# Kernel optimization log

Measured on AMD Instinct MI355X. Metric: run time of the kernel, lower is better.

The kernel has to match this reference:

```python
import jax, jax.numpy as jnp
import numpy as np
import math

H = 16  # num heads
NEG = -1e9


def setup_inputs() -> dict:
    key = jax.random.key(0)
    ks = jax.random.split(key, 12)
    B, S, D = 2, 2048, 1024
    inp = {
        "query": jax.random.normal(ks[0], (B, S, D), jnp.float32),
        "key": jax.random.normal(ks[1], (B, S, D), jnp.float32),
        "value": jax.random.normal(ks[2], (B, S, D), jnp.float32),
        "mask": jax.random.randint(ks[3], (B, 1, S), 0, 2, jnp.int32),
        "wq": jax.random.normal(ks[4], (D, D), jnp.float32) * 0.02,
        "bq": jnp.zeros((D,), jnp.float32),
        "wk": jax.random.normal(ks[5], (D, D), jnp.float32) * 0.02,
        "bk": jnp.zeros((D,), jnp.float32),
        "wv": jax.random.normal(ks[6], (D, D), jnp.float32) * 0.02,
        "bv": jnp.zeros((D,), jnp.float32),
        "wo": jax.random.normal(ks[7], (D, D), jnp.float32) * 0.02,
        "bo": jnp.zeros((D,), jnp.float32),
    }
    return inp


def reference(query, key, value, mask, wq, bq, wk, bk, wv, bv, wo, bo):
    B, S, D = query.shape
    dk = D // H

    def proj(x, w, b):
        # torch Linear: x @ w.T + b ; then split heads -> [B, H, S, dk]
        y = x @ w.T + b
        return y.reshape(B, -1, H, dk).transpose(0, 2, 1, 3)

    q = proj(query, wq, bq)
    k = proj(key, wk, bk)
    v = proj(value, wv, bv)

    scores = jnp.einsum("bhqd,bhkd->bhqk", q, k) / math.sqrt(dk)  # [B,H,S,S]

    m = mask[:, None, :, :]  # [B,1,1,S] (mask.unsqueeze(1) in torch)
    scores = jnp.where(m == 0, NEG, scores)            # key-side padding mask
    scores = jnp.where(jnp.swapaxes(m, -2, -1) == 0, NEG, scores)  # query-side mask (q_len>1)

    p_attn = jax.nn.softmax(scores, axis=-1)
    # dropout p=0 / eval mode -> identity
    ctx = jnp.einsum("bhqk,bhkd->bhqd", p_attn, v)  # [B,H,S,dk]
    ctx = ctx.transpose(0, 2, 1, 3).reshape(B, S, H * dk)
    out = ctx @ wo.T + bo
    return out
```

## Files before the change

### kernel.cpp

```cpp
#include <hip/hip_runtime.h>
#include <hip/hip_bf16.h>

#define SEQ 2048
#define DIM 1024
#define NH  16
#define DK  64
#define NA  (2 * SEQ * DIM)
#define NW  (DIM * DIM)
#define PSTR 72
#define ESTR 136
#define FSTR 132
#define QSCALE 0.18033688011112042f

typedef __attribute__((ext_vector_type(4))) float f32x4;
typedef __attribute__((ext_vector_type(8))) __bf16 bf16x8;
typedef __attribute__((ext_vector_type(4))) __bf16 bf16x4;

__device__ __forceinline__ f32x4 mfma16(bf16x8 a, bf16x8 b, f32x4 c) {
  return __builtin_amdgcn_mfma_f32_16x16x32_bf16(a, b, c, 0, 0, 0);
}
__device__ __forceinline__ void async_load16(const void* g, void* l) {
  __builtin_amdgcn_global_load_lds(
      (const __attribute__((address_space(1))) void*)g,
      (__attribute__((address_space(3))) void*)l, 16, 0, 0);
}
__device__ __forceinline__ int swz(int row, int chunk) {
  return row * 8 + (chunk ^ (row & 7));
}

__global__ __launch_bounds__(256) void cvt_kernel(
    const float* __restrict__ s0, const float* __restrict__ s1,
    const float* __restrict__ s2, const float* __restrict__ s3,
    const float* __restrict__ s4, const float* __restrict__ s5,
    const float* __restrict__ s6,
    __hip_bfloat16* __restrict__ d0, __hip_bfloat16* __restrict__ d1,
    __hip_bfloat16* __restrict__ d2, __hip_bfloat16* __restrict__ d3,
    __hip_bfloat16* __restrict__ d4, __hip_bfloat16* __restrict__ d5,
    __hip_bfloat16* __restrict__ d6) {
  const int id = blockIdx.x;
  const float* s;
  __hip_bfloat16* d;
  int bid;
  if (id < 6144) {
    int t = id >> 11;
    bid = id & 2047;
    s = (t == 0) ? s0 : ((t == 1) ? s1 : s2);
    d = (t == 0) ? d0 : ((t == 1) ? d1 : d2);
  } else {
    int t = (id - 6144) >> 9;
    bid = (id - 6144) & 511;
    s = (t == 0) ? s3 : ((t == 1) ? s4 : ((t == 2) ? s5 : s6));
    d = (t == 0) ? d3 : ((t == 1) ? d4 : ((t == 2) ? d5 : d6));
  }
  size_t i = ((size_t)bid * 256 + threadIdx.x) * 8;
  float4 a = *(const float4*)(s + i);
  float4 b = *(const float4*)(s + i + 4);
  bf16x8 v = {(__bf16)a.x, (__bf16)a.y, (__bf16)a.z, (__bf16)a.w,
              (__bf16)b.x, (__bf16)b.y, (__bf16)b.z, (__bf16)b.w};
  *(bf16x8*)(d + i) = v;
}

__device__ __forceinline__ void gemm_stage(
    const __hip_bfloat16* __restrict__ X, const __hip_bfloat16* __restrict__ W,
    __hip_bfloat16* A, __hip_bfloat16* B, int m0, int n0, int k0,
    int w, int lane) {
  for (int r = 0; r < 4; ++r) {
    int cbase = r * 256 + w * 64;
    int c = cbase + lane, row = c >> 3, cs = c & 7;
    int off = cs ^ (row & 7);
    async_load16((const char*)(X + (size_t)(m0 + row) * DIM + k0) + off * 16,
                 (char*)A + cbase * 16);
    async_load16((const char*)(W + (size_t)(n0 + row) * DIM + k0) + off * 16,
                 (char*)B + cbase * 16);
  }
}

__device__ __forceinline__ void gemm_mainloop(
    const __hip_bfloat16* __restrict__ X, const __hip_bfloat16* __restrict__ W,
    __hip_bfloat16* lds, int m0, int n0, f32x4 acc[4][4]) {
  const int tid = threadIdx.x, lane = tid & 63, w = tid >> 6;
  const int quad = lane >> 4, l15 = lane & 15;
  const int wm = (w >> 1) * 64, wn = (w & 1) * 64;

  f32x4 z = {0.f, 0.f, 0.f, 0.f};
  for (int mi = 0; mi < 4; ++mi)
    for (int ni = 0; ni < 4; ++ni) acc[mi][ni] = z;

  gemm_stage(X, W, lds, lds + 8192, m0, n0, 0, w, lane);
  __syncthreads();

  for (int it = 0; it < 16; ++it) {
    __hip_bfloat16* Ac = lds + (it & 1) * 16384;
    __hip_bfloat16* Bc = Ac + 8192;
    if (it < 15) {
      __hip_bfloat16* An = lds + ((it + 1) & 1) * 16384;
      gemm_stage(X, W, An, An + 8192, m0, n0, (it + 1) * 64, w, lane);
    }
    for (int kk = 0; kk < 2; ++kk) {
      bf16x8 a[4], b[4];
      for (int mi = 0; mi < 4; ++mi)
        a[mi] = *(const bf16x8*)(Ac + swz(wm + mi * 16 + l15, kk * 4 + quad) * 8);
      for (int ni = 0; ni < 4; ++ni)
        b[ni] = *(const bf16x8*)(Bc + swz(wn + ni * 16 + l15, kk * 4 + quad) * 8);
      for (int mi = 0; mi < 4; ++mi)
        for (int ni = 0; ni < 4; ++ni)
          acc[mi][ni] = mfma16(a[mi], b[ni], acc[mi][ni]);
    }
    __syncthreads();
  }
}

__global__ __launch_bounds__(256) void qkv_proj_kernel(
    const __hip_bfloat16* __restrict__ xq, const __hip_bfloat16* __restrict__ xk,
    const __hip_bfloat16* __restrict__ xv,
    const __hip_bfloat16* __restrict__ wq, const __hip_bfloat16* __restrict__ wk,
    const __hip_bfloat16* __restrict__ wv,
    const float* __restrict__ bq, const float* __restrict__ bk,
    const float* __restrict__ bv,
    __hip_bfloat16* __restrict__ q_ws, __hip_bfloat16* __restrict__ k_ws,
    __hip_bfloat16* __restrict__ vt_ws) {
  __shared__ __align__(16) __hip_bfloat16 S_lds[4 * 8192];

  const int z = blockIdx.z;
  const __hip_bfloat16* X = (z == 0) ? xq : ((z == 1) ? xk : xv);
  const __hip_bfloat16* W = (z == 0) ? wq : ((z == 1) ? wk : wv);
  const float* bias = (z == 0) ? bq : ((z == 1) ? bk : bv);
  const float f = (z == 0) ? QSCALE : 1.0f;

  const int m0 = blockIdx.y * 128, n0 = blockIdx.x * 128;
  f32x4 acc[4][4];
  gemm_mainloop(X, W, S_lds, m0, n0, acc);

  const int tid = threadIdx.x, lane = tid & 63, w = tid >> 6;
  const int quad = lane >> 4, l15 = lane & 15;
  const int wm = (w >> 1) * 64, wn = (w & 1) * 64;

  if (z != 2) {
    __hip_bfloat16* out = (z == 0) ? q_ws : k_ws;
    for (int mi = 0; mi < 4; ++mi)
      for (int ni = 0; ni < 4; ++ni) {
        const float bv_ = bias[n0 + wn + ni * 16 + l15];
        for (int r = 0; r < 4; ++r)
          S_lds[(wm + mi * 16 + quad * 4 + r) * ESTR + wn + ni * 16 + l15] =
              __float2bfloat16((acc[mi][ni][r] + bv_) * f);
      }
    __syncthreads();
    for (int r2 = 0; r2 < 8; ++r2) {
      int c = r2 * 256 + tid;
      int row = c >> 4, j = c & 15;
      int m = m0 + row, b = m >> 11, s = m & 2047;
      int n = n0 + j * 8, h = n >> 6, d = n & 63;
      *(uint4*)(out + ((size_t)(b * NH + h) * SEQ + s) * DK + d) =
          *(const uint4*)(S_lds + row * ESTR + j * 8);
    }
  } else {
    for (int mi = 0; mi < 4; ++mi)
      for (int ni = 0; ni < 4; ++ni) {
        const int n_local = wn + ni * 16 + l15;
        const float bv_ = bias[n0 + n_local];
        bf16x4 tv;
        for (int r = 0; r < 4; ++r) tv[r] = (__bf16)(acc[mi][ni][r] + bv_);
        *(bf16x4*)(S_lds + n_local * ESTR + wm + mi * 16 + quad * 4) = tv;
      }
    __syncthreads();
    const int b = m0 >> 11, s_base = m0 & 2047;
    for (int r2 = 0; r2 < 8; ++r2) {
      int c2 = r2 * 256 + tid;
      int nrow = c2 >> 4, moff = (c2 & 15) * 8;
      int n = n0 + nrow, h = n >> 6, d = n & 63;
      *(uint4*)(vt_ws + ((size_t)(b * NH + h) * DK + d) * SEQ + s_base + moff) =
          *(const uint4*)(S_lds + nrow * ESTR + moff);
    }
  }
}

__global__ __launch_bounds__(256) void attn_kernel(
    const __hip_bfloat16* __restrict__ qg, const __hip_bfloat16* __restrict__ kg,
    const __hip_bfloat16* __restrict__ vtg, const int* __restrict__ mask,
    __hip_bfloat16* __restrict__ ctx) {
  __shared__ __align__(16) __hip_bfloat16 QP_lds[128 * PSTR];
  __shared__ __align__(16) __hip_bfloat16 K_lds[2][64 * 64];
  __shared__ __align__(16) __hip_bfloat16 V_lds[2][64 * 64];
  __shared__ float bias_lds[SEQ];

  const int tid = threadIdx.x, lane = tid & 63, w = tid >> 6;
  const int quad = lane >> 4, l15 = lane & 15;
  const int bh = blockIdx.y, b = bh >> 4, h = bh & 15;
  const int q0 = blockIdx.x * 128;
  const size_t head = (size_t)bh * SEQ * DK;
  const size_t vthead = (size_t)bh * DK * SEQ;

  for (int i = tid; i < SEQ; i += 256)
    bias_lds[i] = mask[b * SEQ + i] ? 0.f : -1e9f;

  for (int r = 0; r < 4; ++r) {
    int cbase = r * 256 + w * 64;
    int c = cbase + lane, row = c >> 3, cs = c & 7;
    int off = cs ^ (row & 7);
    async_load16((const char*)(qg + head + (size_t)(q0 + row) * DK) + off * 16,
                 (char*)QP_lds + cbase * 16);
  }
  for (int r = 0; r < 2; ++r) {
    int cbase = r * 256 + w * 64;
    int c = cbase + lane, row = c >> 3, cs = c & 7;
    int off = cs ^ (row & 7);
    async_load16((const char*)(kg + head + (size_t)row * DK) + off * 16,
                 (char*)K_lds[0] + cbase * 16);
    async_load16((const char*)(vtg + vthead + (size_t)row * SEQ) + off * 16,
                 (char*)V_lds[0] + cbase * 16);
  }
  __syncthreads();

  bf16x8 qf[2][2];
  for (int kk = 0; kk < 2; ++kk)
    for (int ni = 0; ni < 2; ++ni)
      qf[kk][ni] = *(const bf16x8*)(QP_lds + swz(w * 32 + ni * 16 + l15, kk * 4 + quad) * 8);
  int qmv[2];
  for (int ni = 0; ni < 2; ++ni)
    qmv[ni] = mask[b * SEQ + q0 + w * 32 + ni * 16 + l15];

  __hip_bfloat16* P_lds = QP_lds;
  const bf16x8 ones = {(__bf16)1.f, (__bf16)1.f, (__bf16)1.f, (__bf16)1.f,
                       (__bf16)1.f, (__bf16)1.f, (__bf16)1.f, (__bf16)1.f};

  f32x4 z = {0.f, 0.f, 0.f, 0.f};
  f32x4 o_acc[2][4];
  for (int ni = 0; ni < 2; ++ni)
    for (int di = 0; di < 4; ++di) o_acc[ni][di] = z;
  f32x4 o_sum[2] = {z, z};

  for (int t = 0; t < 32; ++t) {
    const int cur = t & 1;
    if (t < 31) {
      const int k1 = (t + 1) * 64;
      for (int r = 0; r < 2; ++r) {
        int cbase = r * 256 + w * 64;
        int c = cbase + lane, row = c >> 3, cs = c & 7;
        int off = cs ^ (row & 7);
        async_load16((const char*)(kg + head + (size_t)(k1 + row) * DK) + off * 16,
                     (char*)K_lds[1 - cur] + cbase * 16);
        async_load16((const char*)(vtg + vthead + (size_t)row * SEQ + k1) + off * 16,
                     (char*)V_lds[1 - cur] + cbase * 16);
      }
    }
    const int k0 = t * 64;

    f32x4 s_acc[4][2];
    for (int mi = 0; mi < 4; ++mi) {
      f32x4 kb = *(const f32x4*)(bias_lds + k0 + mi * 16 + quad * 4);
      for (int ni = 0; ni < 2; ++ni) s_acc[mi][ni] = kb;
    }
    for (int kk = 0; kk < 2; ++kk) {
      bf16x8 ak[4];
      for (int mi = 0; mi < 4; ++mi)
        ak[mi] = *(const bf16x8*)(K_lds[cur] + swz(mi * 16 + l15, kk * 4 + quad) * 8);
      for (int mi = 0; mi < 4; ++mi)
        for (int ni = 0; ni < 2; ++ni)
          s_acc[mi][ni] = mfma16(ak[mi], qf[kk][ni], s_acc[mi][ni]);
    }

    for (int mi = 0; mi < 4; ++mi)
      for (int ni = 0; ni < 2; ++ni) {
        bf16x4 pk;
        for (int r = 0; r < 4; ++r) {
          float s2 = qmv[ni] ? s_acc[mi][ni][r] : 0.f;
          pk[r] = (__bf16)__builtin_amdgcn_exp2f(s2);
        }
        *(bf16x4*)(P_lds + (w * 32 + ni * 16 + l15) * PSTR + mi * 16 + quad * 4) = pk;
      }

    for (int kk = 0; kk < 2; ++kk) {
      bf16x8 av[4], bp[2];
      for (int di = 0; di < 4; ++di)
        av[di] = *(const bf16x8*)(V_lds[cur] + swz(di * 16 + l15, kk * 4 + quad) * 8);
      for (int ni = 0; ni < 2; ++ni)
        bp[ni] = *(const bf16x8*)(P_lds + (w * 32 + ni * 16 + l15) * PSTR + kk * 32 + quad * 8);
      for (int ni = 0; ni < 2; ++ni) {
        for (int di = 0; di < 4; ++di)
          o_acc[ni][di] = mfma16(av[di], bp[ni], o_acc[ni][di]);
        o_sum[ni] = mfma16(ones, bp[ni], o_sum[ni]);
      }
    }
    __syncthreads();
  }

  const float inv[2] = {1.f / o_sum[0][0], 1.f / o_sum[1][0]};

  for (int ni = 0; ni < 2; ++ni)
    for (int di = 0; di < 4; ++di) {
      bf16x4 ov;
      for (int r = 0; r < 4; ++r) ov[r] = (__bf16)(o_acc[ni][di][r] * inv[ni]);
      *(bf16x4*)(P_lds + (w * 32 + ni * 16 + l15) * PSTR + di * 16 + quad * 4) = ov;
    }
  __syncthreads();
  for (int r = 0; r < 4; ++r) {
    int c = r * 256 + tid, row = c >> 3, off = c & 7;
    *(uint4*)(ctx + (size_t)(b * SEQ + q0 + row) * DIM + h * DK + off * 8) =
        *(const uint4*)(P_lds + row * PSTR + off * 8);
  }
}

__global__ __launch_bounds__(256) void out_proj_kernel(
    const __hip_bfloat16* __restrict__ ctx, const __hip_bfloat16* __restrict__ wo,
    const float* __restrict__ bo, float* __restrict__ out) {
  __shared__ __align__(16) char S_raw[128 * FSTR * 4];
  __hip_bfloat16* S_lds = (__hip_bfloat16*)S_raw;

  const int m0 = blockIdx.y * 128, n0 = blockIdx.x * 128;
  f32x4 acc[4][4];
  gemm_mainloop(ctx, wo, S_lds, m0, n0, acc);

  const int tid = threadIdx.x, lane = tid & 63, w = tid >> 6;
  const int quad = lane >> 4, l15 = lane & 15;
  const int wm = (w >> 1) * 64, wn = (w & 1) * 64;
  float* epi = (float*)S_raw;

  for (int mi = 0; mi < 4; ++mi)
    for (int ni = 0; ni < 4; ++ni) {
      const float bv_ = bo[n0 + wn + ni * 16 + l15];
      for (int r = 0; r < 4; ++r)
        epi[(wm + mi * 16 + quad * 4 + r) * FSTR + wn + ni * 16 + l15] =
            acc[mi][ni][r] + bv_;
    }
  __syncthreads();
  for (int r2 = 0; r2 < 16; ++r2) {
    int c = r2 * 256 + tid;
    int row = c >> 5, j = c & 31;
    *(float4*)(out + (size_t)(m0 + row) * DIM + n0 + j * 4) =
        *(const float4*)(epi + row * FSTR + j * 4);
  }
}

extern "C" void kernel_launch(void* const* d_in, const int* in_sizes, int n_in,
                              void* d_out, int out_size, void* d_ws, size_t ws_size,
                              hipStream_t stream) {
  const float* query = (const float*)d_in[0];
  const float* key   = (const float*)d_in[1];
  const float* value = (const float*)d_in[2];
  const int*   mask  = (const int*)d_in[3];
  const float* wq = (const float*)d_in[4];
  const float* bq = (const float*)d_in[5];
  const float* wk = (const float*)d_in[6];
  const float* bk = (const float*)d_in[7];
  const float* wv = (const float*)d_in[8];
  const float* bv = (const float*)d_in[9];
  const float* wo = (const float*)d_in[10];
  const float* bo = (const float*)d_in[11];
  float* out = (float*)d_out;

  char* ws = (char*)d_ws;
  const size_t SZA = (size_t)NA * 2;
  const size_t SZW = (size_t)NW * 2;
  __hip_bfloat16* xq  = (__hip_bfloat16*)(ws);
  __hip_bfloat16* xk  = (__hip_bfloat16*)(ws + SZA);
  __hip_bfloat16* xv  = (__hip_bfloat16*)(ws + 2 * SZA);
  __hip_bfloat16* wqb = (__hip_bfloat16*)(ws + 3 * SZA);
  __hip_bfloat16* wkb = (__hip_bfloat16*)(ws + 3 * SZA + SZW);
  __hip_bfloat16* wvb = (__hip_bfloat16*)(ws + 3 * SZA + 2 * SZW);
  __hip_bfloat16* wob = (__hip_bfloat16*)(ws + 3 * SZA + 3 * SZW);
  __hip_bfloat16* q_ws  = (__hip_bfloat16*)(ws + 3 * SZA + 4 * SZW);
  __hip_bfloat16* k_ws  = (__hip_bfloat16*)(ws + 4 * SZA + 4 * SZW);
  __hip_bfloat16* vt_ws = (__hip_bfloat16*)(ws + 5 * SZA + 4 * SZW);
  __hip_bfloat16* ctx_ws = xq;

  cvt_kernel<<<dim3(8192), dim3(256), 0, stream>>>(
      query, key, value, wq, wk, wv, wo, xq, xk, xv, wqb, wkb, wvb, wob);
  qkv_proj_kernel<<<dim3(8, 32, 3), dim3(256), 0, stream>>>(
      xq, xk, xv, wqb, wkb, wvb, bq, bk, bv, q_ws, k_ws, vt_ws);
  attn_kernel<<<dim3(16, 32), dim3(256), 0, stream>>>(q_ws, k_ws, vt_ws, mask, ctx_ws);
  out_proj_kernel<<<dim3(8, 32), dim3(256), 0, stream>>>(ctx_ws, wob, bo, out);
}
```

Before: 243.4 us.

## Split attention KV range across two wave halves with LDS reduction

The attention block grows to 512 threads. Each pair of waves handles the same 32 query rows, and each wave in the pair takes one half of the key sequence, so partial outputs and row sums are combined through LDS at the end. The mask-to-bias conversion moves into an extra block of the conversion kernel and is read from global memory, and Q fragments are loaded directly from global instead of staged through LDS. The aim is more waves in flight per block for better latency hiding. In exchange, the K/V double buffering is dropped in favour of a load-then-sync per iteration, which exposes load latency and adds a reduction step.

Result: faster. 223.3 us (-8.2%).

```diff
diff --git a/kernel.cpp b/kernel.cpp
--- a/kernel.cpp
+++ b/kernel.cpp
@@ -32,12 +32,17 @@
     const float* __restrict__ s0, const float* __restrict__ s1,
     const float* __restrict__ s2, const float* __restrict__ s3,
     const float* __restrict__ s4, const float* __restrict__ s5,
-    const float* __restrict__ s6,
+    const float* __restrict__ s6, const int* __restrict__ mask,
     __hip_bfloat16* __restrict__ d0, __hip_bfloat16* __restrict__ d1,
     __hip_bfloat16* __restrict__ d2, __hip_bfloat16* __restrict__ d3,
     __hip_bfloat16* __restrict__ d4, __hip_bfloat16* __restrict__ d5,
-    __hip_bfloat16* __restrict__ d6) {
+    __hip_bfloat16* __restrict__ d6, float* __restrict__ biasg) {
   const int id = blockIdx.x;
+  if (id == 8192) {
+    for (int i = threadIdx.x; i < 2 * SEQ; i += 256)
+      biasg[i] = mask[i] ? 0.f : -1e9f;
+    return;
+  }
   const float* s;
   __hip_bfloat16* d;
   int bid;
@@ -174,86 +179,72 @@
   }
 }
 
-__global__ __launch_bounds__(256) void attn_kernel(
+__global__ __launch_bounds__(512, 4) void attn_kernel(
     const __hip_bfloat16* __restrict__ qg, const __hip_bfloat16* __restrict__ kg,
     const __hip_bfloat16* __restrict__ vtg, const int* __restrict__ mask,
-    __hip_bfloat16* __restrict__ ctx) {
-  __shared__ __align__(16) __hip_bfloat16 QP_lds[128 * PSTR];
-  __shared__ __align__(16) __hip_bfloat16 K_lds[2][64 * 64];
-  __shared__ __align__(16) __hip_bfloat16 V_lds[2][64 * 64];
-  __shared__ float bias_lds[SEQ];
+    const float* __restrict__ biasg, __hip_bfloat16* __restrict__ ctx) {
+  __shared__ __align__(16) char KV_raw[32768];
+  __shared__ __align__(16) __hip_bfloat16 P_lds[256 * PSTR];
+  __shared__ float osum_lds[4][32];
+
+  __hip_bfloat16* K_lds = (__hip_bfloat16*)KV_raw;
+  __hip_bfloat16* V_lds = (__hip_bfloat16*)(KV_raw + 16384);
 
   const int tid = threadIdx.x, lane = tid & 63, w = tid >> 6;
   const int quad = lane >> 4, l15 = lane & 15;
+  const int g = w >> 1, half = w & 1;
   const int bh = blockIdx.y, b = bh >> 4, h = bh & 15;
   const int q0 = blockIdx.x * 128;
   const size_t head = (size_t)bh * SEQ * DK;
   const size_t vthead = (size_t)bh * DK * SEQ;
 
-  for (int i = tid; i < SEQ; i += 256)
-    bias_lds[i] = mask[b * SEQ + i] ? 0.f : -1e9f;
-
-  for (int r = 0; r < 4; ++r) {
-    int cbase = r * 256 + w * 64;
-    int c = cbase + lane, row = c >> 3, cs = c & 7;
-    int off = cs ^ (row & 7);
-    async_load16((const char*)(qg + head + (size_t)(q0 + row) * DK) + off * 16,
-                 (char*)QP_lds + cbase * 16);
-  }
-  for (int r = 0; r < 2; ++r) {
-    int cbase = r * 256 + w * 64;
-    int c = cbase + lane, row = c >> 3, cs = c & 7;
-    int off = cs ^ (row & 7);
-    async_load16((const char*)(kg + head + (size_t)row * DK) + off * 16,
-                 (char*)K_lds[0] + cbase * 16);
-    async_load16((const char*)(vtg + vthead + (size_t)row * SEQ) + off * 16,
-                 (char*)V_lds[0] + cbase * 16);
-  }
-  __syncthreads();
-
   bf16x8 qf[2][2];
   for (int kk = 0; kk < 2; ++kk)
     for (int ni = 0; ni < 2; ++ni)
-      qf[kk][ni] = *(const bf16x8*)(QP_lds + swz(w * 32 + ni * 16 + l15, kk * 4 + quad) * 8);
+      qf[kk][ni] = *(const bf16x8*)(qg + head +
+          (size_t)(q0 + g * 32 + ni * 16 + l15) * DK + kk * 32 + quad * 8);
   int qmv[2];
   for (int ni = 0; ni < 2; ++ni)
-    qmv[ni] = mask[b * SEQ + q0 + w * 32 + ni * 16 + l15];
-
-  __hip_bfloat16* P_lds = QP_lds;
+    qmv[ni] = mask[b * SEQ + q0 + g * 32 + ni * 16 + l15];
+  const float* bias_b = biasg + b * SEQ;
+
   const bf16x8 ones = {(__bf16)1.f, (__bf16)1.f, (__bf16)1.f, (__bf16)1.f,
                        (__bf16)1.f, (__bf16)1.f, (__bf16)1.f, (__bf16)1.f};
-
   f32x4 z = {0.f, 0.f, 0.f, 0.f};
   f32x4 o_acc[2][4];
   for (int ni = 0; ni < 2; ++ni)
     for (int di = 0; di < 4; ++di) o_acc[ni][di] = z;
   f32x4 o_sum[2] = {z, z};
-
-  for (int t = 0; t < 32; ++t) {
-    const int cur = t & 1;
-    if (t < 31) {
-      const int k1 = (t + 1) * 64;
-      for (int r = 0; r < 2; ++r) {
-        int cbase = r * 256 + w * 64;
-        int c = cbase + lane, row = c >> 3, cs = c & 7;
-        int off = cs ^ (row & 7);
-        async_load16((const char*)(kg + head + (size_t)(k1 + row) * DK) + off * 16,
-                     (char*)K_lds[1 - cur] + cbase * 16);
-        async_load16((const char*)(vtg + vthead + (size_t)row * SEQ + k1) + off * 16,
-                     (char*)V_lds[1 - cur] + cbase * 16);
-      }
-    }
-    const int k0 = t * 64;
+  __hip_bfloat16* P_w = P_lds + w * 32 * PSTR;
+
+  for (int u = 0; u < 16; ++u) {
+    {
+      int row = tid >> 3, cs = tid & 7;
+      int off = cs ^ (row & 7);
+      async_load16((const char*)(kg + head + (size_t)(u * 64 + row) * DK) + off * 16,
+                   (char*)K_lds + tid * 16);
+      async_load16((const char*)(kg + head + (size_t)((16 + u) * 64 + row) * DK) + off * 16,
+                   (char*)(K_lds + 4096) + tid * 16);
+      async_load16((const char*)(vtg + vthead + (size_t)row * SEQ + u * 64) + off * 16,
+                   (char*)V_lds + tid * 16);
+      async_load16((const char*)(vtg + vthead + (size_t)row * SEQ + (16 + u) * 64) + off * 16,
+                   (char*)(V_lds + 4096) + tid * 16);
+    }
+    __syncthreads();
+
+    const __hip_bfloat16* Kc = K_lds + half * 4096;
+    const __hip_bfloat16* Vc = V_lds + half * 4096;
+    const int kbase = (half * 16 + u) * 64;
 
     f32x4 s_acc[4][2];
     for (int mi = 0; mi < 4; ++mi) {
-      f32x4 kb = *(const f32x4*)(bias_lds + k0 + mi * 16 + quad * 4);
+      f32x4 kb = *(const f32x4*)(bias_b + kbase + mi * 16 + quad * 4);
       for (int ni = 0; ni < 2; ++ni) s_acc[mi][ni] = kb;
     }
     for (int kk = 0; kk < 2; ++kk) {
       bf16x8 ak[4];
       for (int mi = 0; mi < 4; ++mi)
-        ak[mi] = *(const bf16x8*)(K_lds[cur] + swz(mi * 16 + l15, kk * 4 + quad) * 8);
+        ak[mi] = *(const bf16x8*)(Kc + swz(mi * 16 + l15, kk * 4 + quad) * 8);
       for (int mi = 0; mi < 4; ++mi)
         for (int ni = 0; ni < 2; ++ni)
           s_acc[mi][ni] = mfma16(ak[mi], qf[kk][ni], s_acc[mi][ni]);
@@ -266,15 +257,15 @@
           float s2 = qmv[ni] ? s_acc[mi][ni][r] : 0.f;
           pk[r] = (__bf16)__builtin_amdgcn_exp2f(s2);
         }
-        *(bf16x4*)(P_lds + (w * 32 + ni * 16 + l15) * PSTR + mi * 16 + quad * 4) = pk;
+        *(bf16x4*)(P_w + (ni * 16 + l15) * PSTR + mi * 16 + quad * 4) = pk;
       }
 
     for (int kk = 0; kk < 2; ++kk) {
       bf16x8 av[4], bp[2];
       for (int di = 0; di < 4; ++di)
-        av[di] = *(const bf16x8*)(V_lds[cur] + swz(di * 16 + l15, kk * 4 + quad) * 8);
+        av[di] = *(const bf16x8*)(Vc + swz(di * 16 + l15, kk * 4 + quad) * 8);
       for (int ni = 0; ni < 2; ++ni)
-        bp[ni] = *(const bf16x8*)(P_lds + (w * 32 + ni * 16 + l15) * PSTR + kk * 32 + quad * 8);
+        bp[ni] = *(const bf16x8*)(P_w + (ni * 16 + l15) * PSTR + kk * 32 + quad * 8);
       for (int ni = 0; ni < 2; ++ni) {
         for (int di = 0; di < 4; ++di)
           o_acc[ni][di] = mfma16(av[di], bp[ni], o_acc[ni][di]);
@@ -284,17 +275,35 @@
     __syncthreads();
   }
 
-  const float inv[2] = {1.f / o_sum[0][0], 1.f / o_sum[1][0]};
-
-  for (int ni = 0; ni < 2; ++ni)
-    for (int di = 0; di < 4; ++di) {
-      bf16x4 ov;
-      for (int r = 0; r < 4; ++r) ov[r] = (__bf16)(o_acc[ni][di][r] * inv[ni]);
-      *(bf16x4*)(P_lds + (w * 32 + ni * 16 + l15) * PSTR + di * 16 + quad * 4) = ov;
-    }
+  float* scr = (float*)KV_raw;
+  if (half == 0) {
+    for (int ni = 0; ni < 2; ++ni)
+      for (int di = 0; di < 4; ++di) {
+        int row = g * 32 + ni * 16 + l15, ch = di * 4 + quad;
+        *(f32x4*)(scr + (row * 16 + (ch ^ (row & 7))) * 4) = o_acc[ni][di];
+      }
+    if (quad == 0)
+      for (int ni = 0; ni < 2; ++ni)
+        osum_lds[g][ni * 16 + l15] = o_sum[ni][0];
+  }
   __syncthreads();
-  for (int r = 0; r < 4; ++r) {
-    int c = r * 256 + tid, row = c >> 3, off = c & 7;
+  if (half == 1) {
+    float inv[2];
+    for (int ni = 0; ni < 2; ++ni)
+      inv[ni] = 1.f / (o_sum[ni][0] + osum_lds[g][ni * 16 + l15]);
+    for (int ni = 0; ni < 2; ++ni)
+      for (int di = 0; di < 4; ++di) {
+        int row = g * 32 + ni * 16 + l15, ch = di * 4 + quad;
+        f32x4 part = *(const f32x4*)(scr + (row * 16 + (ch ^ (row & 7))) * 4);
+        bf16x4 ov;
+        for (int r = 0; r < 4; ++r)
+          ov[r] = (__bf16)((o_acc[ni][di][r] + part[r]) * inv[ni]);
+        *(bf16x4*)(P_lds + row * PSTR + di * 16 + quad * 4) = ov;
+      }
+  }
+  __syncthreads();
+  for (int r = 0; r < 2; ++r) {
+    int c = r * 512 + tid, row = c >> 3, off = c & 7;
     *(uint4*)(ctx + (size_t)(b * SEQ + q0 + row) * DIM + h * DK + off * 8) =
         *(const uint4*)(P_lds + row * PSTR + off * 8);
   }
@@ -361,12 +370,15 @@
   __hip_bfloat16* q_ws  = (__hip_bfloat16*)(ws + 3 * SZA + 4 * SZW);
   __hip_bfloat16* k_ws  = (__hip_bfloat16*)(ws + 4 * SZA + 4 * SZW);
   __hip_bfloat16* vt_ws = (__hip_bfloat16*)(ws + 5 * SZA + 4 * SZW);
+  float* biasg = (float*)(ws + 6 * SZA + 4 * SZW);
   __hip_bfloat16* ctx_ws = xq;
 
-  cvt_kernel<<<dim3(8192), dim3(256), 0, stream>>>(
-      query, key, value, wq, wk, wv, wo, xq, xk, xv, wqb, wkb, wvb, wob);
+  cvt_kernel<<<dim3(8193), dim3(256), 0, stream>>>(
+      query, key, value, wq, wk, wv, wo, mask,
+      xq, xk, xv, wqb, wkb, wvb, wob, biasg);
   qkv_proj_kernel<<<dim3(8, 32, 3), dim3(256), 0, stream>>>(
       xq, xk, xv, wqb, wkb, wvb, bq, bk, bv, q_ws, k_ws, vt_ws);
-  attn_kernel<<<dim3(16, 32), dim3(256), 0, stream>>>(q_ws, k_ws, vt_ws, mask, ctx_ws);
+  attn_kernel<<<dim3(16, 32), dim3(512), 0, stream>>>(
+      q_ws, k_ws, vt_ws, mask, biasg, ctx_ws);
   out_proj_kernel<<<dim3(8, 32), dim3(256), 0, stream>>>(ctx_ws, wob, bo, out);
 }
```
